# Kernel tuning notes

Hardware: AMD Instinct MI355X
Metric: run time of the kernel (lower is better)

Reference implementation:

```python
import jax, jax.numpy as jnp
import numpy as np

ALPHA = 0.2  # LeakyReLU negative slope
N, IN_DIM, OUT_DIM = 8192, 512, 64


def setup_inputs() -> dict:
    key = jax.random.key(0)
    k1, k2, k3, k4 = jax.random.split(key, 4)
    X = jax.random.normal(k1, (N, IN_DIM), dtype=jnp.float32)
    Adj = jax.random.randint(k2, (N, N), 0, 2, dtype=jnp.int32)
    # xavier_uniform with gain=1.414
    def xavier(k, shape, gain=1.414):
        fan_in, fan_out = shape[0], shape[1]
        bound = gain * np.sqrt(6.0 / (fan_in + fan_out))
        return jax.random.uniform(k, shape, jnp.float32, -bound, bound)
    W = xavier(k3, (IN_DIM, OUT_DIM))
    a = xavier(k4, (2 * OUT_DIM, 1))
    return {"X": X, "Adj": Adj, "W": W, "a": a}


def reference(X, Adj, W, a):
    # h = X @ W : [N, D]
    h = X @ W
    D = h.shape[1]
    # Decompose pairwise score: concat([h_i, h_j]) @ a == h_i @ a1 + h_j @ a2
    s1 = h @ a[:D, 0]   # [N] -- contribution of row (destination) node i
    s2 = h @ a[D:, 0]   # [N] -- contribution of column (source) node j
    e = jnp.exp(jax.nn.leaky_relu(s1[:, None] + s2[None, :], negative_slope=ALPHA))  # [N, N]
    e = jnp.where(Adj == 0, jnp.float32(0.0), e)
    attention = e / jnp.sum(e, axis=1, keepdims=True)
    # dropout is a no-op in eval mode (training=False)
    return attention @ h
```

## Files before the change

kernel.cpp:

```cpp
#include <hip/hip_runtime.h>
#include <math.h>


#define NN 8192
#define KIN 512
#define DD 64
#define ALPHA 0.2f

using floatx4 = __attribute__((ext_vector_type(4))) float;
using bf16x8  = __attribute__((ext_vector_type(8))) __bf16;

__global__ __launch_bounds__(256) void k_gemm_h(const float* __restrict__ X,
                                                const float* __restrict__ W,
                                                float* __restrict__ h) {
    __shared__ __align__(16) float XT[32 * 36];
    __shared__ __align__(16) float WL[32 * 64];
    const int t = threadIdx.x;
    const int i0 = blockIdx.x * 32;
    const int rb = t >> 5;
    const int db = t & 31;
    float acc[4][2] = {};

    for (int k0 = 0; k0 < KIN; k0 += 32) {
        {
            const int row = t >> 3, kq = t & 7;
            const float4 x4 = *(const float4*)(X + (size_t)(i0 + row) * KIN + k0 + kq * 4);
            XT[(kq * 4 + 0) * 36 + row] = x4.x;
            XT[(kq * 4 + 1) * 36 + row] = x4.y;
            XT[(kq * 4 + 2) * 36 + row] = x4.z;
            XT[(kq * 4 + 3) * 36 + row] = x4.w;
#pragma unroll
            for (int p = 0; p < 2; ++p) {
                const int q = p * 256 + t;
                const int kk = q >> 4, dq = q & 15;
                *(float4*)(WL + kk * 64 + dq * 4) =
                    *(const float4*)(W + (size_t)(k0 + kk) * DD + dq * 4);
            }
        }
        __syncthreads();
#pragma unroll
        for (int k = 0; k < 32; ++k) {
            const float4 xa = *(const float4*)(XT + k * 36 + rb * 4);
            const float2 wb = *(const float2*)(WL + k * 64 + db * 2);
            const float xv[4] = {xa.x, xa.y, xa.z, xa.w};
#pragma unroll
            for (int i = 0; i < 4; ++i) {
                acc[i][0] += xv[i] * wb.x;
                acc[i][1] += xv[i] * wb.y;
            }
        }
        __syncthreads();
    }
#pragma unroll
    for (int i = 0; i < 4; ++i) {
        float2 o = {acc[i][0], acc[i][1]};
        *(float2*)(h + (size_t)(i0 + rb * 4 + i) * DD + db * 2) = o;
    }
}

__global__ __launch_bounds__(256) void k_s12(const float* __restrict__ h,
                                             const float* __restrict__ a,
                                             float* __restrict__ s1,
                                             float* __restrict__ s2) {
    const int lane = threadIdx.x & 63;
    const int w = threadIdx.x >> 6;
    const int r = blockIdx.x * 4 + w;
    const float v = h[(size_t)r * DD + lane];
    float p1 = v * a[lane];
    float p2 = v * a[64 + lane];
#pragma unroll
    for (int off = 32; off; off >>= 1) {
        p1 += __shfl_xor(p1, off, 64);
        p2 += __shfl_xor(p2, off, 64);
    }
    if (lane == 0) {
        s1[r] = p1;
        s2[r] = p2;
    }
}

__global__ __launch_bounds__(256) void k_hfrag(const float* __restrict__ h,
                                               __bf16* __restrict__ hFrag) {
    const int f = blockIdx.x * 256 + threadIdx.x;
    const int lane = f & 63, dt = (f >> 6) & 3, jblk = f >> 8;
    const int n = lane & 15, q = lane >> 4;
    bf16x8 v;
#pragma unroll
    for (int jj = 0; jj < 8; ++jj)
        v[jj] = (__bf16)h[(size_t)(jblk * 32 + q * 8 + jj) * DD + dt * 16 + n];
    *(bf16x8*)(hFrag + (size_t)f * 8) = v;
}

__global__ __launch_bounds__(256) void k_pack(const int* __restrict__ Adj,
                                              unsigned int* __restrict__ mask) {
    const int lane = threadIdx.x & 63;
    const int wid = (blockIdx.x * 256 + threadIdx.x) >> 6;
    const int nw = (gridDim.x * 256) >> 6;
    for (int it = wid; it < (NN * NN / 512); it += nw) {
        const size_t base = (size_t)it * 512;
        unsigned long long m[8];
#pragma unroll
        for (int p = 0; p < 8; ++p) {
            const int v = Adj[base + (size_t)p * 64 + lane];
            m[p] = __ballot(v != 0);
        }
        if (lane == 0) {
            unsigned long long* o = (unsigned long long*)mask + (size_t)it * 8;
#pragma unroll
            for (int p = 0; p < 8; ++p) o[p] = m[p];
        }
    }
}

__global__ __launch_bounds__(256, 4) void k_attn4(const bf16x8* __restrict__ hFrag,
                                                  const unsigned int* __restrict__ mask,
                                                  const float* __restrict__ s1,
                                                  const float* __restrict__ s2,
                                                  float* __restrict__ numP,
                                                  float* __restrict__ denP) {
    const int t = threadIdx.x;
    const int wv = t >> 6;
    const int lane = t & 63;
    const int n = lane & 15, q = lane >> 4;
    const int it = blockIdx.x >> 3, jc = blockIdx.x & 7;
    const int i0 = it * 64;
    const int row = i0 + wv * 16 + n;
    const float s1v = s1[row];

    unsigned int mr[32];
    {
        const uint4* mp = (const uint4*)(mask + (size_t)row * 256 + jc * 32);
#pragma unroll
        for (int p = 0; p < 8; ++p) {
            const uint4 v = mp[p];
            mr[p * 4 + 0] = v.x;
            mr[p * 4 + 1] = v.y;
            mr[p * 4 + 2] = v.z;
            mr[p * 4 + 3] = v.w;
        }
    }

    bf16x8 ones;
#pragma unroll
    for (int u = 0; u < 8; ++u) ones[u] = (__bf16)1.0f;

    floatx4 acc[5] = {};
    const int jbase = jc * 1024;

#pragma unroll
    for (int ks = 0; ks < 32; ++ks) {
        const int j0 = jbase + ks * 32 + q * 8;
        const float4 z0 = *(const float4*)(s2 + j0);
        const float4 z1 = *(const float4*)(s2 + j0 + 4);
        const unsigned int bits = (mr[ks] >> (q * 8)) & 0xffu;
        const float zz[8] = {z0.x, z0.y, z0.z, z0.w, z1.x, z1.y, z1.z, z1.w};
        bf16x8 af;
#pragma unroll
        for (int u = 0; u < 8; ++u) {
            const float s = s1v + zz[u];
            const float l = fmaxf(s, ALPHA * s);
            const float e = (bits & (1u << u)) ? __expf(l) : 0.f;
            af[u] = (__bf16)e;
        }
        const bf16x8* hf = hFrag + ((size_t)(jc * 32 + ks) * 4) * 64 + lane;
#pragma unroll
        for (int dt = 0; dt < 4; ++dt)
            acc[dt] = __builtin_amdgcn_mfma_f32_16x16x32_bf16(af, hf[dt * 64], acc[dt], 0, 0, 0);
        acc[4] = __builtin_amdgcn_mfma_f32_16x16x32_bf16(af, ones, acc[4], 0, 0, 0);
    }

    const size_t base = (size_t)blockIdx.x * 4096;
#pragma unroll
    for (int dt = 0; dt < 4; ++dt)
#pragma unroll
        for (int r = 0; r < 4; ++r)
            numP[base + (size_t)(wv * 16 + q * 4 + r) * 64 + dt * 16 + n] = acc[dt][r];

    if (n == 0) {
#pragma unroll
        for (int r = 0; r < 4; ++r)
            denP[(size_t)blockIdx.x * 64 + wv * 16 + q * 4 + r] = acc[4][r];
    }
}

__global__ __launch_bounds__(256) void k_final(const float* __restrict__ numP,
                                               const float* __restrict__ denP,
                                               float* __restrict__ out) {
    const int idx = blockIdx.x * 256 + threadIdx.x;
    const int i = idx >> 6, d = idx & 63;
    const int it = i >> 6, r = i & 63;
    float num = 0.f, den = 0.f;
#pragma unroll
    for (int c = 0; c < 8; ++c) {
        const size_t bx = (size_t)(it * 8 + c);
        num += numP[bx * 4096 + (size_t)r * 64 + d];
        den += denP[bx * 64 + r];
    }
    out[idx] = num / den;
}

extern "C" void kernel_launch(void* const* d_in, const int* in_sizes, int n_in,
                              void* d_out, int out_size, void* d_ws, size_t ws_size,
                              hipStream_t stream) {
    const float* X = (const float*)d_in[0];
    const int* Adj = (const int*)d_in[1];
    const float* W = (const float*)d_in[2];
    const float* a = (const float*)d_in[3];
    float* out = (float*)d_out;

    float* ws = (float*)d_ws;
    float* h = ws;
    float* s1 = h + 524288;
    float* s2 = s1 + 8192;
    __bf16* hFrag = (__bf16*)(s2 + 8192);
    unsigned int* mask = (unsigned int*)(s2 + 8192 + 262144);
    float* numP = s2 + 8192 + 262144 + 2097152;
    float* denP = numP + 1024 * 4096;

    k_pack<<<2048, 256, 0, stream>>>(Adj, mask);
    k_gemm_h<<<256, 256, 0, stream>>>(X, W, h);
    k_s12<<<2048, 256, 0, stream>>>(h, a, s1, s2);
    k_hfrag<<<256, 256, 0, stream>>>(h, hFrag);
    k_attn4<<<1024, 256, 0, stream>>>((const bf16x8*)hFrag, mask, s1, s2, numP, denP);
    k_final<<<2048, 256, 0, stream>>>(numP, denP, out);
}
```

Measured before the change: 445.0 us.

## Fuse projection GEMM, score vectors and bf16 fragment packing into one kernel

The X@W GEMM kernel now keeps its 32-row h tile in shared memory and computes s1/s2 and the bf16 MFMA fragment layout for hFrag in the same kernel. This removes the h round-trip through global memory and two kernel launches. The attention kernel also stops preloading all 32 mask words into registers and instead loads 8 words per outer iteration in a non-unrolled loop. That lowers register pressure but adds per-iteration load latency.

```diff
diff --git a/kernel.cpp b/kernel.cpp
--- a/kernel.cpp
+++ b/kernel.cpp
@@ -10,11 +10,16 @@
 using floatx4 = __attribute__((ext_vector_type(4))) float;
 using bf16x8  = __attribute__((ext_vector_type(8))) __bf16;
 
-__global__ __launch_bounds__(256) void k_gemm_h(const float* __restrict__ X,
-                                                const float* __restrict__ W,
-                                                float* __restrict__ h) {
-    __shared__ __align__(16) float XT[32 * 36];
-    __shared__ __align__(16) float WL[32 * 64];
+__global__ __launch_bounds__(256) void k_fused(const float* __restrict__ X,
+                                               const float* __restrict__ W,
+                                               const float* __restrict__ a,
+                                               float* __restrict__ s1,
+                                               float* __restrict__ s2,
+                                               __bf16* __restrict__ hFrag) {
+    __shared__ __align__(16) float smem[3200];
+    float* XT = smem;
+    float* WL = smem + 32 * 36;
+    float* hT = smem;
     const int t = threadIdx.x;
     const int i0 = blockIdx.x * 32;
     const int rb = t >> 5;
@@ -53,42 +58,39 @@
     }
 #pragma unroll
     for (int i = 0; i < 4; ++i) {
-        float2 o = {acc[i][0], acc[i][1]};
-        *(float2*)(h + (size_t)(i0 + rb * 4 + i) * DD + db * 2) = o;
-    }
-}
-
-__global__ __launch_bounds__(256) void k_s12(const float* __restrict__ h,
-                                             const float* __restrict__ a,
-                                             float* __restrict__ s1,
-                                             float* __restrict__ s2) {
-    const int lane = threadIdx.x & 63;
-    const int w = threadIdx.x >> 6;
-    const int r = blockIdx.x * 4 + w;
-    const float v = h[(size_t)r * DD + lane];
-    float p1 = v * a[lane];
-    float p2 = v * a[64 + lane];
-#pragma unroll
-    for (int off = 32; off; off >>= 1) {
-        p1 += __shfl_xor(p1, off, 64);
-        p2 += __shfl_xor(p2, off, 64);
-    }
-    if (lane == 0) {
-        s1[r] = p1;
-        s2[r] = p2;
-    }
-}
-
-__global__ __launch_bounds__(256) void k_hfrag(const float* __restrict__ h,
-                                               __bf16* __restrict__ hFrag) {
-    const int f = blockIdx.x * 256 + threadIdx.x;
-    const int lane = f & 63, dt = (f >> 6) & 3, jblk = f >> 8;
-    const int n = lane & 15, q = lane >> 4;
-    bf16x8 v;
-#pragma unroll
-    for (int jj = 0; jj < 8; ++jj)
-        v[jj] = (__bf16)h[(size_t)(jblk * 32 + q * 8 + jj) * DD + dt * 16 + n];
-    *(bf16x8*)(hFrag + (size_t)f * 8) = v;
+        hT[(rb * 4 + i) * 66 + db * 2 + 0] = acc[i][0];
+        hT[(rb * 4 + i) * 66 + db * 2 + 1] = acc[i][1];
+    }
+    __syncthreads();
+    {
+        const int r = t >> 3, sub = t & 7;
+        float p1 = 0.f, p2 = 0.f;
+#pragma unroll
+        for (int u = 0; u < 8; ++u) {
+            const int d = sub * 8 + u;
+            const float v = hT[r * 66 + d];
+            p1 += v * a[d];
+            p2 += v * a[64 + d];
+        }
+#pragma unroll
+        for (int off = 1; off < 8; off <<= 1) {
+            p1 += __shfl_xor(p1, off, 64);
+            p2 += __shfl_xor(p2, off, 64);
+        }
+        if (sub == 0) {
+            s1[i0 + r] = p1;
+            s2[i0 + r] = p2;
+        }
+    }
+    {
+        const int lane = t & 63, dt = t >> 6;
+        const int n = lane & 15, q = lane >> 4;
+        bf16x8 v;
+#pragma unroll
+        for (int jj = 0; jj < 8; ++jj)
+            v[jj] = (__bf16)hT[(q * 8 + jj) * 66 + dt * 16 + n];
+        *(bf16x8*)(hFrag + ((size_t)blockIdx.x * 256 + t) * 8) = v;
+    }
 }
 
 __global__ __launch_bounds__(256) void k_pack(const int* __restrict__ Adj,
@@ -112,7 +114,7 @@
     }
 }
 
-__global__ __launch_bounds__(256, 4) void k_attn4(const bf16x8* __restrict__ hFrag,
+__global__ __launch_bounds__(256, 4) void k_attn5(const bf16x8* __restrict__ hFrag,
                                                   const unsigned int* __restrict__ mask,
                                                   const float* __restrict__ s1,
                                                   const float* __restrict__ s2,
@@ -126,47 +128,42 @@
     const int i0 = it * 64;
     const int row = i0 + wv * 16 + n;
     const float s1v = s1[row];
-
-    unsigned int mr[32];
-    {
-        const uint4* mp = (const uint4*)(mask + (size_t)row * 256 + jc * 32);
-#pragma unroll
-        for (int p = 0; p < 8; ++p) {
-            const uint4 v = mp[p];
-            mr[p * 4 + 0] = v.x;
-            mr[p * 4 + 1] = v.y;
-            mr[p * 4 + 2] = v.z;
-            mr[p * 4 + 3] = v.w;
-        }
-    }
+    const unsigned int* mrow = mask + (size_t)row * 256 + jc * 32;
+    const int jbase = jc * 1024;
 
     bf16x8 ones;
 #pragma unroll
     for (int u = 0; u < 8; ++u) ones[u] = (__bf16)1.0f;
 
     floatx4 acc[5] = {};
-    const int jbase = jc * 1024;
-
-#pragma unroll
-    for (int ks = 0; ks < 32; ++ks) {
-        const int j0 = jbase + ks * 32 + q * 8;
-        const float4 z0 = *(const float4*)(s2 + j0);
-        const float4 z1 = *(const float4*)(s2 + j0 + 4);
-        const unsigned int bits = (mr[ks] >> (q * 8)) & 0xffu;
-        const float zz[8] = {z0.x, z0.y, z0.z, z0.w, z1.x, z1.y, z1.z, z1.w};
-        bf16x8 af;
-#pragma unroll
-        for (int u = 0; u < 8; ++u) {
-            const float s = s1v + zz[u];
-            const float l = fmaxf(s, ALPHA * s);
-            const float e = (bits & (1u << u)) ? __expf(l) : 0.f;
-            af[u] = (__bf16)e;
-        }
-        const bf16x8* hf = hFrag + ((size_t)(jc * 32 + ks) * 4) * 64 + lane;
-#pragma unroll
-        for (int dt = 0; dt < 4; ++dt)
-            acc[dt] = __builtin_amdgcn_mfma_f32_16x16x32_bf16(af, hf[dt * 64], acc[dt], 0, 0, 0);
-        acc[4] = __builtin_amdgcn_mfma_f32_16x16x32_bf16(af, ones, acc[4], 0, 0, 0);
+
+#pragma unroll 1
+    for (int o = 0; o < 4; ++o) {
+        const uint4 mA = *(const uint4*)(mrow + o * 8);
+        const uint4 mB = *(const uint4*)(mrow + o * 8 + 4);
+        const unsigned int mr[8] = {mA.x, mA.y, mA.z, mA.w, mB.x, mB.y, mB.z, mB.w};
+#pragma unroll
+        for (int k8 = 0; k8 < 8; ++k8) {
+            const int ks = o * 8 + k8;
+            const int j0 = jbase + ks * 32 + q * 8;
+            const float4 z0 = *(const float4*)(s2 + j0);
+            const float4 z1 = *(const float4*)(s2 + j0 + 4);
+            const unsigned int bits = (mr[k8] >> (q * 8)) & 0xffu;
+            const float zz[8] = {z0.x, z0.y, z0.z, z0.w, z1.x, z1.y, z1.z, z1.w};
+            bf16x8 af;
+#pragma unroll
+            for (int u = 0; u < 8; ++u) {
+                const float s = s1v + zz[u];
+                const float l = fmaxf(s, ALPHA * s);
+                const float e = (bits & (1u << u)) ? __expf(l) : 0.f;
+                af[u] = (__bf16)e;
+            }
+            const bf16x8* hf = hFrag + ((size_t)(jc * 32 + ks) * 4) * 64 + lane;
+#pragma unroll
+            for (int dt = 0; dt < 4; ++dt)
+                acc[dt] = __builtin_amdgcn_mfma_f32_16x16x32_bf16(af, hf[dt * 64], acc[dt], 0, 0, 0);
+            acc[4] = __builtin_amdgcn_mfma_f32_16x16x32_bf16(af, ones, acc[4], 0, 0, 0);
+        }
     }
 
     const size_t base = (size_t)blockIdx.x * 4096;
@@ -209,18 +206,15 @@
     float* out = (float*)d_out;
 
     float* ws = (float*)d_ws;
-    float* h = ws;
-    float* s1 = h + 524288;
+    float* s1 = ws;
     float* s2 = s1 + 8192;
     __bf16* hFrag = (__bf16*)(s2 + 8192);
     unsigned int* mask = (unsigned int*)(s2 + 8192 + 262144);
-    float* numP = s2 + 8192 + 262144 + 2097152;
+    float* numP = (float*)(s2 + 8192 + 262144 + 2097152);
     float* denP = numP + 1024 * 4096;
 
+    k_fused<<<256, 256, 0, stream>>>(X, W, a, s1, s2, hFrag);
     k_pack<<<2048, 256, 0, stream>>>(Adj, mask);
-    k_gemm_h<<<256, 256, 0, stream>>>(X, W, h);
-    k_s12<<<2048, 256, 0, stream>>>(h, a, s1, s2);
-    k_hfrag<<<256, 256, 0, stream>>>(h, hFrag);
-    k_attn4<<<1024, 256, 0, stream>>>((const bf16x8*)hFrag, mask, s1, s2, numP, denP);
+    k_attn5<<<1024, 256, 0, stream>>>((const bf16x8*)hFrag, mask, s1, s2, numP, denP);
     k_final<<<2048, 256, 0, stream>>>(numP, denP, out);
 }
```

New measurement: 445.1 us. About the same (+0.0%).
